# Optimization experiments

Measured on AMD Instinct MI355X. Metric: run time of the kernel, lower is better.

The kernel has to match this reference:

```python
import jax, jax.numpy as jnp
import numpy as np

BS = 16
CTX_PER = 1024   # local context nodes per proof state
ARGS_PER = 32    # arguments per proof state
KEY_DIM = 128
D_MODEL = 512


def setup_inputs() -> dict:
    key = jax.random.key(0)
    k1, k2, k3 = jax.random.split(key, 3)
    n_ctx = BS * CTX_PER
    n_args = BS * ARGS_PER
    # segment ids: sorted, uniform segments (static ragged structure)
    ctx_ids = jnp.repeat(jnp.arange(BS, dtype=jnp.int32), CTX_PER)
    arg_ids = jnp.repeat(jnp.arange(BS, dtype=jnp.int32), ARGS_PER)
    arg_values = jax.random.normal(k1, (n_args, KEY_DIM), dtype=jnp.float32)
    ctx_values = jax.random.normal(k2, (n_ctx, D_MODEL), dtype=jnp.float32)
    W = jax.random.normal(k3, (D_MODEL, KEY_DIM), dtype=jnp.float32) / np.sqrt(D_MODEL)
    b = jnp.zeros((KEY_DIM,), dtype=jnp.float32)
    return {"bs": BS, "arg_ids": arg_ids, "ctx_ids": ctx_ids,
            "arg_values": arg_values, "ctx_values": ctx_values, "W": W, "b": b}


def reference(bs, arg_ids, ctx_ids, arg_values, ctx_values, W, b):
    n_args = arg_ids.shape[0]
    n_ctx = ctx_ids.shape[0]
    # total (arg, ctx-element) pairs; static because segments are uniform by construction
    P = n_args * (n_ctx // bs)

    # ctx_lens[s] = number of context elements in proof state s
    ctx_lens = jax.ops.segment_sum(jnp.ones_like(ctx_ids), ctx_ids, num_segments=bs)
    arg_ctx_lens = ctx_lens[arg_ids]                      # [n_args]

    # ragged-range construction: row id + within-row offset for each flat pair
    arg_ends = jnp.cumsum(arg_ctx_lens)                   # inclusive cumsum
    arg_starts = arg_ends - arg_ctx_lens                  # exclusive cumsum
    pos = jnp.arange(P, dtype=arg_ends.dtype)
    rows = jnp.searchsorted(arg_ends, pos, side='right')  # value_rowids  [P]
    offs = pos - arg_starts[rows]                         # ragged range values [P]

    # column index into flat context values
    ctx_starts = jnp.cumsum(ctx_lens) - ctx_lens          # exclusive cumsum [bs]
    cols = ctx_starts[arg_ids[rows]] + offs               # [P]

    keys_all = ctx_values @ W + b                         # Dense key projection [n_ctx, key_dim]
    queries = arg_values[rows]                            # [P, key_dim]
    keys = keys_all[cols]                                 # [P, key_dim]
    logits_flat = jnp.einsum('pd,pd->p', queries, keys)   # [P]
    return rows.astype(jnp.int32), logits_flat
```

## Files before the change

kernel.cpp:

```cpp
#include <hip/hip_runtime.h>


#define BSZ        16
#define CTX_PER    1024
#define ARGS_PER   32
#define KD         128
#define DM         512
#define N_ARGS     (BSZ * ARGS_PER)
#define P_TOTAL    (N_ARGS * CTX_PER)

typedef __attribute__((ext_vector_type(8))) short short8;
typedef __attribute__((ext_vector_type(4))) float float4v;

__device__ inline short bf16_of(float x) {
    unsigned u = __builtin_bit_cast(unsigned, x);
    unsigned r = (u + 0x7fffu + ((u >> 16) & 1u)) >> 16;
    return (short)r;
}

__device__ inline short8 cvt8(float4 lo, float4 hi) {
    short8 r;
    r[0] = bf16_of(lo.x); r[1] = bf16_of(lo.y); r[2] = bf16_of(lo.z); r[3] = bf16_of(lo.w);
    r[4] = bf16_of(hi.x); r[5] = bf16_of(hi.y); r[6] = bf16_of(hi.z); r[7] = bf16_of(hi.w);
    return r;
}

__global__ __launch_bounds__(256) void qproj_kernel(
    const float* __restrict__ arg, const float* __restrict__ W,
    const float* __restrict__ b, short* __restrict__ Qp, float* __restrict__ qb)
{
    const int t = threadIdx.x, lane = t & 63, wave = t >> 6;
    const int mtile = blockIdx.x >> 3;
    const int ntile = (blockIdx.x & 7) * 4 + wave;
    const int n = lane & 15, quad = lane >> 4;

    const float* asrc = arg + (size_t)(mtile * 16 + n) * KD + quad * 8;
    short8 afr[4];
    #pragma unroll
    for (int kt = 0; kt < 4; ++kt)
        afr[kt] = cvt8(*(const float4*)(asrc + kt * 32), *(const float4*)(asrc + kt * 32 + 4));

    const float* wsrc = W + (size_t)(ntile * 16 + n) * KD + quad * 8;
    float4v acc = {0.f, 0.f, 0.f, 0.f};
    #pragma unroll
    for (int kt = 0; kt < 4; ++kt) {
        short8 bfr = cvt8(*(const float4*)(wsrc + kt * 32), *(const float4*)(wsrc + kt * 32 + 4));
        acc = __builtin_amdgcn_mfma_f32_16x16x32_bf16(afr[kt], bfr, acc, 0, 0, 0);
    }
    #pragma unroll
    for (int r = 0; r < 4; ++r)
        Qp[(size_t)(mtile * 16 + quad * 4 + r) * DM + ntile * 16 + n] = bf16_of(acc[r]);

    if ((blockIdx.x & 7) == 0) {
        __shared__ float red[16][17];
        const int al = t >> 4, seg = t & 15;
        const float* qrow = arg + (size_t)(mtile * 16 + al) * KD + seg * 8;
        float p = 0.f;
        #pragma unroll
        for (int j = 0; j < 8; ++j) p += qrow[j] * b[seg * 8 + j];
        red[al][seg] = p;
        __syncthreads();
        if (t < 16) {
            float ssum = 0.f;
            #pragma unroll
            for (int j = 0; j < 16; ++j) ssum += red[t][j];
            qb[mtile * 16 + t] = ssum;
        }
    }
}

__global__ __launch_bounds__(256, 2) void main_kernel(
    const float* __restrict__ ctx, const short* __restrict__ Qp,
    const float* __restrict__ qb, float* __restrict__ out)
{
    __shared__ __align__(16) short Qpl[32][520];

    const int t = threadIdx.x, lane = t & 63, wave = t >> 6;
    const int s = blockIdx.x >> 5;
    const int chunk = blockIdx.x & 31;

    const int n = lane & 15, quad = lane >> 4;
    const int A16 = (wave & 1) * 16;
    const int rowbase = chunk * 32 + ((wave >> 1) & 1) * 16;

    const float* csrc = ctx + (size_t)(s * CTX_PER + rowbase + n) * DM + quad * 8;

    const float4 c0lo = *(const float4*)(csrc);
    const float4 c0hi = *(const float4*)(csrc + 4);
    const float4 c1lo = *(const float4*)(csrc + 32);
    const float4 c1hi = *(const float4*)(csrc + 36);

    const short* qsrc = Qp + (size_t)s * 32 * DM;
    #pragma unroll
    for (int i = 0; i < 8; ++i) {
        const int u = i * 256 + t;
        const int row = u >> 6, c = u & 63;
        *(float4*)&Qpl[row][c * 8] = *(const float4*)(qsrc + (size_t)row * DM + c * 8);
    }

    {
        const int a = t >> 3, c4 = (t & 7) * 4;
        const int ga = s * ARGS_PER + a;
        const float gaf = (float)ga;
        float4 rv = make_float4(gaf, gaf, gaf, gaf);
        *(float4*)(out + (size_t)ga * CTX_PER + chunk * 32 + c4) = rv;
    }

    __syncthreads();

    const short* qrow = &Qpl[A16 + n][quad * 8];

    float4v acc = {0.f, 0.f, 0.f, 0.f};
    {
        short8 a0 = *(const short8*)(qrow);
        acc = __builtin_amdgcn_mfma_f32_16x16x32_bf16(a0, cvt8(c0lo, c0hi), acc, 0, 0, 0);
        short8 a1 = *(const short8*)(qrow + 32);
        acc = __builtin_amdgcn_mfma_f32_16x16x32_bf16(a1, cvt8(c1lo, c1hi), acc, 0, 0, 0);
    }
    #pragma unroll
    for (int kt = 2; kt < 16; ++kt) {
        const float4 lo = *(const float4*)(csrc + kt * 32);
        const float4 hi = *(const float4*)(csrc + kt * 32 + 4);
        short8 bfr = cvt8(lo, hi);
        short8 a  = *(const short8*)(qrow + kt * 32);
        acc = __builtin_amdgcn_mfma_f32_16x16x32_bf16(a, bfr, acc, 0, 0, 0);
    }

    const int ga0 = s * ARGS_PER + A16 + quad * 4;
    const float4 qv = *(const float4*)(qb + ga0);
    float* obase = out + P_TOTAL + (size_t)ga0 * CTX_PER + rowbase + n;
    obase[0]           = acc[0] + qv.x;
    obase[CTX_PER]     = acc[1] + qv.y;
    obase[2 * CTX_PER] = acc[2] + qv.z;
    obase[3 * CTX_PER] = acc[3] + qv.w;
}

extern "C" void kernel_launch(void* const* d_in, const int* in_sizes, int n_in,
                              void* d_out, int out_size, void* d_ws, size_t ws_size,
                              hipStream_t stream)
{
    const float* arg_values = (const float*)d_in[3];
    const float* ctx_values = (const float*)d_in[4];
    const float* W          = (const float*)d_in[5];
    const float* b          = (const float*)d_in[6];
    float* out = (float*)d_out;

    short* Qp = (short*)d_ws;
    float* qb = (float*)((char*)d_ws + (size_t)N_ARGS * DM * sizeof(short));

    qproj_kernel<<<256, 256, 0, stream>>>(arg_values, W, b, Qp, qb);
    main_kernel<<<BSZ * 32, 256, 0, stream>>>(ctx_values, Qp, qb, out);
}
```

Baseline: 93.55 us.

## Drop LDS staging of Q, shrink blocks, use packed bf16 conversion

The main kernel no longer stages the 32x512 bf16 query tile in shared memory behind a barrier. Each wave now reads its query fragments straight from global memory (expected to hit L2), and the grid becomes 1024 blocks of 128 threads covering 16 context rows each. The hand-written float-to-bf16 rounding is replaced by the HIP __float22bfloat162_rn intrinsic, which may map to a packed conversion instruction. The aim is to remove the barrier and LDS round trip and to improve latency hiding, at the cost of roughly doubling query reads through L2.

```diff
diff --git a/kernel.cpp b/kernel.cpp
--- a/kernel.cpp
+++ b/kernel.cpp
@@ -1,4 +1,5 @@
 #include <hip/hip_runtime.h>
+#include <hip/hip_bf16.h>
 
 
 #define BSZ        16
@@ -19,10 +20,12 @@
 }
 
 __device__ inline short8 cvt8(float4 lo, float4 hi) {
-    short8 r;
-    r[0] = bf16_of(lo.x); r[1] = bf16_of(lo.y); r[2] = bf16_of(lo.z); r[3] = bf16_of(lo.w);
-    r[4] = bf16_of(hi.x); r[5] = bf16_of(hi.y); r[6] = bf16_of(hi.z); r[7] = bf16_of(hi.w);
-    return r;
+    union { short8 s; __hip_bfloat162 h[4]; } u;
+    u.h[0] = __float22bfloat162_rn(make_float2(lo.x, lo.y));
+    u.h[1] = __float22bfloat162_rn(make_float2(lo.z, lo.w));
+    u.h[2] = __float22bfloat162_rn(make_float2(hi.x, hi.y));
+    u.h[3] = __float22bfloat162_rn(make_float2(hi.z, hi.w));
+    return u.s;
 }
 
 __global__ __launch_bounds__(256) void qproj_kernel(
@@ -69,66 +72,41 @@
     }
 }
 
-__global__ __launch_bounds__(256, 2) void main_kernel(
+__global__ void main_kernel(
     const float* __restrict__ ctx, const short* __restrict__ Qp,
     const float* __restrict__ qb, float* __restrict__ out)
 {
-    __shared__ __align__(16) short Qpl[32][520];
-
     const int t = threadIdx.x, lane = t & 63, wave = t >> 6;
-    const int s = blockIdx.x >> 5;
-    const int chunk = blockIdx.x & 31;
+    const int s = blockIdx.x >> 6;
+    const int chunk = blockIdx.x & 63;
 
     const int n = lane & 15, quad = lane >> 4;
-    const int A16 = (wave & 1) * 16;
-    const int rowbase = chunk * 32 + ((wave >> 1) & 1) * 16;
+    const int A16 = wave * 16;
 
-    const float* csrc = ctx + (size_t)(s * CTX_PER + rowbase + n) * DM + quad * 8;
-
-    const float4 c0lo = *(const float4*)(csrc);
-    const float4 c0hi = *(const float4*)(csrc + 4);
-    const float4 c1lo = *(const float4*)(csrc + 32);
-    const float4 c1hi = *(const float4*)(csrc + 36);
-
-    const short* qsrc = Qp + (size_t)s * 32 * DM;
-    #pragma unroll
-    for (int i = 0; i < 8; ++i) {
-        const int u = i * 256 + t;
-        const int row = u >> 6, c = u & 63;
-        *(float4*)&Qpl[row][c * 8] = *(const float4*)(qsrc + (size_t)row * DM + c * 8);
+    {
+        const int a = t >> 2, c4 = (t & 3) * 4;
+        const int ga = s * ARGS_PER + a;
+        const float gaf = (float)ga;
+        *(float4*)(out + (size_t)ga * CTX_PER + chunk * 16 + c4) =
+            make_float4(gaf, gaf, gaf, gaf);
     }
 
-    {
-        const int a = t >> 3, c4 = (t & 7) * 4;
-        const int ga = s * ARGS_PER + a;
-        const float gaf = (float)ga;
-        float4 rv = make_float4(gaf, gaf, gaf, gaf);
-        *(float4*)(out + (size_t)ga * CTX_PER + chunk * 32 + c4) = rv;
-    }
-
-    __syncthreads();
-
-    const short* qrow = &Qpl[A16 + n][quad * 8];
+    const float* csrc = ctx + (size_t)(s * CTX_PER + chunk * 16 + n) * DM + quad * 8;
+    const short* qsrc = Qp + (size_t)(s * 32 + A16 + n) * DM + quad * 8;
 
     float4v acc = {0.f, 0.f, 0.f, 0.f};
-    {
-        short8 a0 = *(const short8*)(qrow);
-        acc = __builtin_amdgcn_mfma_f32_16x16x32_bf16(a0, cvt8(c0lo, c0hi), acc, 0, 0, 0);
-        short8 a1 = *(const short8*)(qrow + 32);
-        acc = __builtin_amdgcn_mfma_f32_16x16x32_bf16(a1, cvt8(c1lo, c1hi), acc, 0, 0, 0);
-    }
     #pragma unroll
-    for (int kt = 2; kt < 16; ++kt) {
+    for (int kt = 0; kt < 16; ++kt) {
         const float4 lo = *(const float4*)(csrc + kt * 32);
         const float4 hi = *(const float4*)(csrc + kt * 32 + 4);
         short8 bfr = cvt8(lo, hi);
-        short8 a  = *(const short8*)(qrow + kt * 32);
+        short8 a   = *(const short8*)(qsrc + kt * 32);
         acc = __builtin_amdgcn_mfma_f32_16x16x32_bf16(a, bfr, acc, 0, 0, 0);
     }
 
     const int ga0 = s * ARGS_PER + A16 + quad * 4;
     const float4 qv = *(const float4*)(qb + ga0);
-    float* obase = out + P_TOTAL + (size_t)ga0 * CTX_PER + rowbase + n;
+    float* obase = out + P_TOTAL + (size_t)ga0 * CTX_PER + chunk * 16 + n;
     obase[0]           = acc[0] + qv.x;
     obase[CTX_PER]     = acc[1] + qv.y;
     obase[2 * CTX_PER] = acc[2] + qv.z;
@@ -149,5 +127,5 @@
     float* qb = (float*)((char*)d_ws + (size_t)N_ARGS * DM * sizeof(short));
 
     qproj_kernel<<<256, 256, 0, stream>>>(arg_values, W, b, Qp, qb);
-    main_kernel<<<BSZ * 32, 256, 0, stream>>>(ctx_values, Qp, qb, out);
+    main_kernel<<<BSZ * 64, 128, 0, stream>>>(ctx_values, Qp, qb, out);
 }
```

After: 99.30 us. 6.1% more time.
